# Optimization experiments

Measured on AMD Instinct MI355X. Metric: run time of the kernel, lower is better.

The kernel has to match this reference:

```python
import jax, jax.numpy as jnp
from jax import lax
import numpy as np

CH = 16      # channel_n
HID = 128    # update MLP width


def setup_inputs() -> dict:
    key = jax.random.key(0)
    ks = jax.random.split(key, 7)
    B, H, W = 4, 224, 224
    x = jax.random.uniform(ks[0], (B, CH, H, W), dtype=jnp.float32)
    # perception: Conv2d(16 -> 48, 3x3, pad 1, no bias), OIHW
    w_percep = jax.random.normal(ks[1], (CH * 3, CH, 3, 3), jnp.float32) * 0.05
    # update MLP: 1x1 convs == pointwise linears over channels
    w1 = jax.random.normal(ks[2], (HID, CH * 3), jnp.float32) * 0.05
    b1 = jax.random.normal(ks[3], (HID,), jnp.float32) * 0.01
    w2 = jax.random.normal(ks[4], (HID, HID), jnp.float32) * 0.05
    b2 = jax.random.normal(ks[5], (HID,), jnp.float32) * 0.01
    w3 = jax.random.normal(ks[6], (CH, HID), jnp.float32) * 0.05  # no bias
    return {"x": x, "w_percep": w_percep, "w1": w1, "b1": b1,
            "w2": w2, "b2": b2, "w3": w3, "steps": 40}


def reference(x, w_percep, w1, b1, w2, b2, w3, steps):
    dn = ("NCHW", "OIHW", "NCHW")

    def step(x, _):
        # 3x3 perception conv, same padding  -> [B, 48, H, W]
        p = lax.conv_general_dilated(x, w_percep, (1, 1), "SAME",
                                     dimension_numbers=dn)
        # pointwise conv-MLP (1x1 convs as channel einsums)
        h = jax.nn.relu(jnp.einsum("bchw,oc->bohw", p, w1) + b1[None, :, None, None])
        h = jax.nn.relu(jnp.einsum("bchw,oc->bohw", h, w2) + b2[None, :, None, None])
        dx = jnp.einsum("bchw,oc->bohw", h, w3)
        # residual update + clamp to [0, 1] (eval mode: no fire mask)
        return jnp.clip(x + dx, 0.0, 1.0), None

    x, _ = lax.scan(step, x, None, length=steps)
    return x
```

## Files before the change

### kernel.cpp

```cpp
#include <hip/hip_runtime.h>


typedef __attribute__((ext_vector_type(8))) short short8;
typedef __attribute__((ext_vector_type(4))) float float4v;
typedef __attribute__((ext_vector_type(2))) float float2v;

#define MFMA16(a, b, c) __builtin_amdgcn_mfma_f32_16x16x32_bf16((a), (b), (c), 0, 0, 0)

__device__ __forceinline__ short f2bf(float f) {
  unsigned u = __builtin_bit_cast(unsigned, f);
  return (short)((u + 0x8000u) >> 16);
}

__device__ __forceinline__ unsigned pk2bf(float a, float b) {
#if __has_builtin(__builtin_amdgcn_cvt_pk_bf16_f32)
  typedef __attribute__((ext_vector_type(2))) __bf16 bf2;
  bf2 r = __builtin_amdgcn_cvt_pk_bf16_f32(a, b);
  return __builtin_bit_cast(unsigned, r);
#else
  unsigned ua = __builtin_bit_cast(unsigned, a), ub = __builtin_bit_cast(unsigned, b);
  return ((ua + 0x8000u) >> 16) | (((ub + 0x8000u) >> 16) << 16);
#endif
}

__device__ __forceinline__ void async16(const void* g, void* l) {
  __builtin_amdgcn_global_load_lds((const __attribute__((address_space(1))) void*)g,
                                   (__attribute__((address_space(3))) void*)l,
                                   16, 0, 0);
}

__device__ __forceinline__ void sync_lds() {
  asm volatile("s_waitcnt lgkmcnt(0)\n\ts_barrier" ::: "memory");
}

#define WS_WE    0
#define WS_W2    43008
#define WS_W3    77824
#define WS_B1    82944
#define WS_B2    83456
#define WS_X32A  83968
#define WS_X32B  12929024
#define WS_X16A  25774080
#define WS_X16B  32196608

__global__ void prep_x(const float* __restrict__ x, float* __restrict__ x32,
                       short* __restrict__ x16) {
  int i = blockIdx.x * 256 + threadIdx.x;
  int w = i % 224;
  int h = (i / 224) % 224;
  int c = (i / 50176) & 15;
  int bb = i / 802816;
  float v = x[i];
  int o = ((bb * 224 + h) * 224 + w) * 16 + c;
  x32[o] = v;
  x16[o] = f2bf(v);
}

__global__ void prep_w(const float* __restrict__ wp, const float* __restrict__ w1,
                       const float* __restrict__ b1, const float* __restrict__ w2,
                       const float* __restrict__ b2, const float* __restrict__ w3,
                       short* __restrict__ wE, short* __restrict__ w2t,
                       short* __restrict__ w3t, float* __restrict__ b1p,
                       float* __restrict__ b2p) {
  int i = blockIdx.x * 256 + threadIdx.x;
  if (i < 21504) {
    int o = i / 168, k = i % 168;
    float v = 0.f;
    if (k < 144) {
      int off = k >> 4, c = k & 15;
      for (int c3 = 0; c3 < 48; ++c3)
        v += w1[o * 48 + c3] * wp[c3 * 144 + c * 9 + off];
    }
    wE[i] = f2bf(v);
  } else if (i < 38912) {
    int j = i - 21504;
    int n = j / 136, kk = j % 136;
    float v = 0.f;
    if (kk < 128) { int ch = 16 * (kk & 7) + (kk >> 3); v = w2[n * 128 + ch]; }
    w2t[j] = f2bf(v);
  } else if (i < 41472) {
    int j = i - 38912;
    float v = 0.f;
    if (j < 2176) {
      int n = j / 136, kk = j % 136;
      if (kk < 128) { int ch = 16 * (kk & 7) + (kk >> 3); v = w3[n * 128 + ch]; }
    }
    w3t[j] = f2bf(v);
  } else if (i < 41600) {
    int p = i - 41472;
    b1p[p] = b1[16 * (p & 7) + (p >> 3)];
  } else {
    int p = i - 41600;
    b2p[p] = b2[16 * (p & 7) + (p >> 3)];
  }
}

template <bool LAST>
__global__ __launch_bounds__(512, 4) void ca_step(
    const short* __restrict__ wEg, const short* __restrict__ w2g,
    const short* __restrict__ w3g, const float* __restrict__ b1p,
    const float* __restrict__ b2p, const float* __restrict__ xs32,
    const short* __restrict__ xs16, float* __restrict__ xd32,
    short* __restrict__ xd16, float* __restrict__ dout) {
  __shared__ short sXH[4 * 3616];
  __shared__ short sBUF[2 * 2 * 2176];
  __shared__ short sH2[2 * 2 * 2176];

  const int tid = threadIdx.x;
  const int lane = tid & 63;
  const int wv = tid >> 6;
  const int c16 = lane & 15;
  const int q = lane >> 4;
  const int q8 = q * 8;
  const int qh = q >> 1;
  const int c0 = (q & 1) * 8;

  const int blk = blockIdx.x;
  const int b = blk / 112;
  const int h0 = (blk % 112) * 2;

  const short8 z8 = {0, 0, 0, 0, 0, 0, 0, 0};
  for (int t = wv; t < 28; t += 8) {
    int hr = t / 7, ck = t % 7;
    int hh = h0 - 1 + hr;
    char* l = (char*)sXH + hr * 7232 + 32 + ck * 1024;
    if (hh >= 0 && hh < 224) {
      const char* g = (const char*)xs16 + ((size_t)(b * 224 + hh) * 224) * 32 + ck * 1024;
      async16(g + lane * 16, l);
    } else {
      *(short8*)(l + lane * 16) = z8;
    }
  }
  if (tid < 16) {
    int hr = tid >> 2, wch = tid & 3;
    int colb = (wch < 2) ? 0 : 225;
    *(short8*)((char*)sXH + hr * 7232 + colb * 32 + (wch & 1) * 16) = z8;
  }

  if (wv < 4) {
    const int wq = wv;
    short8 wf[5][2];
#pragma unroll
    for (int kc = 0; kc < 5; ++kc)
#pragma unroll
      for (int n = 0; n < 2; ++n)
        wf[kc][n] = *(const short8*)(wEg + ((2 * wq + n) * 16 + c16) * 168 + kc * 32 + q8);
    const float2v bH = *(const float2v*)(b1p + c16 * 8 + 2 * wq);

    __syncthreads();

    for (int j = 0; j < 16; ++j) {
      if (j < 14) {
        const int t0 = 2 * j, t1 = t0 + 1;
        const int hb0 = ((t0 / 14) * 226 + (t0 % 14) * 16) * 16;
        const int hb1 = ((t1 / 14) * 226 + (t1 % 14) * 16) * 16;
        float4v acc[2][2];
#pragma unroll
        for (int tt = 0; tt < 2; ++tt)
#pragma unroll
          for (int n = 0; n < 2; ++n) acc[tt][n] = (float4v){0.f, 0.f, 0.f, 0.f};
#pragma unroll
        for (int kc = 0; kc < 5; ++kc) {
          int off = kc * 2 + qh;
          if (off > 8) off = 8;
          int dy = (off * 11) >> 5;
          int dxx = off - dy * 3;
          const int ao = (dy * 226 + dxx + c16) * 16 + c0;
          short8 a0 = *(const short8*)(sXH + hb0 + ao);
          short8 a1 = *(const short8*)(sXH + hb1 + ao);
#pragma unroll
          for (int n = 0; n < 2; ++n) {
            acc[0][n] = MFMA16(a0, wf[kc][n], acc[0][n]);
            acc[1][n] = MFMA16(a1, wf[kc][n], acc[1][n]);
          }
        }
#pragma unroll
        for (int tt = 0; tt < 2; ++tt) {
          short* dst = sBUF + ((j & 1) * 2 + tt) * 2176;
#pragma unroll
          for (int r = 0; r < 4; ++r) {
            unsigned d = pk2bf(fmaxf(acc[tt][0][r] + bH[0], 0.f),
                               fmaxf(acc[tt][1][r] + bH[1], 0.f));
            *(unsigned*)(dst + (q * 4 + r) * 136 + c16 * 8 + 2 * wq) = d;
          }
        }
      }
      sync_lds();
    }
  } else {
    const int g = wv - 4;
    short8 w2f[4][2];
    short8 w3f[4];
#pragma unroll
    for (int kc = 0; kc < 4; ++kc)
#pragma unroll
      for (int n = 0; n < 2; ++n)
        w2f[kc][n] = *(const short8*)(w2g + ((2 * g + n) * 16 + c16) * 136 + kc * 32 + q8);
#pragma unroll
    for (int kc = 0; kc < 4; ++kc)
      w3f[kc] = *(const short8*)(w3g + c16 * 136 + kc * 32 + q8);
    const float2v bG = *(const float2v*)(b2p + c16 * 8 + 2 * g);

    __syncthreads();

    for (int j = 0; j < 16; ++j) {
      float xres[4];
      int cb3 = 0, hglob3 = 0;
      if (g < 2 && j >= 2) {
        const int t3 = 2 * (j - 2) + g;
        cb3 = (t3 % 14) * 16; hglob3 = h0 + t3 / 14;
#pragma unroll
        for (int r = 0; r < 4; ++r) {
          size_t pix = (size_t)(b * 224 + hglob3) * 224 + cb3 + q * 4 + r;
          xres[r] = xs32[pix * 16 + c16];
        }
      }
      if (j >= 1 && j <= 14) {
        const short* srcA = sBUF + (((j - 1) & 1) * 2 + 0) * 2176;
        const short* srcB = sBUF + (((j - 1) & 1) * 2 + 1) * 2176;
        float4v acc2[2][2];
#pragma unroll
        for (int tt = 0; tt < 2; ++tt)
#pragma unroll
          for (int n = 0; n < 2; ++n) acc2[tt][n] = (float4v){0.f, 0.f, 0.f, 0.f};
#pragma unroll
        for (int kc = 0; kc < 4; ++kc) {
          short8 aA = *(const short8*)(srcA + c16 * 136 + kc * 32 + q8);
          short8 aB = *(const short8*)(srcB + c16 * 136 + kc * 32 + q8);
#pragma unroll
          for (int n = 0; n < 2; ++n) {
            acc2[0][n] = MFMA16(aA, w2f[kc][n], acc2[0][n]);
            acc2[1][n] = MFMA16(aB, w2f[kc][n], acc2[1][n]);
          }
        }
#pragma unroll
        for (int tt = 0; tt < 2; ++tt) {
          short* dsth2 = sH2 + ((j & 1) * 2 + tt) * 2176;
#pragma unroll
          for (int r = 0; r < 4; ++r) {
            unsigned d = pk2bf(fmaxf(acc2[tt][0][r] + bG[0], 0.f),
                               fmaxf(acc2[tt][1][r] + bG[1], 0.f));
            *(unsigned*)(dsth2 + (q * 4 + r) * 136 + c16 * 8 + 2 * g) = d;
          }
        }
      }
      if (g < 2 && j >= 2) {
        const short* srch2 = sH2 + (((j - 1) & 1) * 2 + g) * 2176;
        float4v acc3 = (float4v){0.f, 0.f, 0.f, 0.f};
#pragma unroll
        for (int kc = 0; kc < 4; ++kc) {
          short8 a = *(const short8*)(srch2 + c16 * 136 + kc * 32 + q8);
          acc3 = MFMA16(a, w3f[kc], acc3);
        }
#pragma unroll
        for (int r = 0; r < 4; ++r) {
          int col = cb3 + q * 4 + r;
          size_t pix = (size_t)(b * 224 + hglob3) * 224 + col;
          float v = xres[r] + acc3[r];
          v = fminf(fmaxf(v, 0.f), 1.f);
          if (LAST) {
            dout[((size_t)(b * 16 + c16) * 224 + hglob3) * 224 + col] = v;
          } else {
            xd32[pix * 16 + c16] = v;
            xd16[pix * 16 + c16] = f2bf(v);
          }
        }
      }
      sync_lds();
    }
  }
}

extern "C" void kernel_launch(void* const* d_in, const int* in_sizes, int n_in,
                              void* d_out, int out_size, void* d_ws, size_t ws_size,
                              hipStream_t stream) {
  const float* x  = (const float*)d_in[0];
  const float* wp = (const float*)d_in[1];
  const float* w1 = (const float*)d_in[2];
  const float* b1 = (const float*)d_in[3];
  const float* w2 = (const float*)d_in[4];
  const float* b2 = (const float*)d_in[5];
  const float* w3 = (const float*)d_in[6];

  char* ws = (char*)d_ws;
  short* wEg = (short*)(ws + WS_WE);
  short* w2g = (short*)(ws + WS_W2);
  short* w3g = (short*)(ws + WS_W3);
  float* b1p = (float*)(ws + WS_B1);
  float* b2p = (float*)(ws + WS_B2);
  float* X32[2] = {(float*)(ws + WS_X32A), (float*)(ws + WS_X32B)};
  short* X16[2] = {(short*)(ws + WS_X16A), (short*)(ws + WS_X16B)};

  prep_x<<<12544, 256, 0, stream>>>(x, X32[0], X16[0]);
  prep_w<<<163, 256, 0, stream>>>(wp, w1, b1, w2, b2, w3, wEg, w2g, w3g, b1p, b2p);

  for (int s = 0; s < 39; ++s) {
    int sb = s & 1;
    ca_step<false><<<448, 512, 0, stream>>>(wEg, w2g, w3g, b1p, b2p,
                                            X32[sb], X16[sb],
                                            X32[1 - sb], X16[1 - sb], nullptr);
  }
  ca_step<true><<<448, 512, 0, stream>>>(wEg, w2g, w3g, b1p, b2p,
                                         X32[1], X16[1],
                                         X32[0], X16[0], (float*)d_out);
}
```

Measured before the change: 1.007 ms.

## Pipeline one 16-pixel tile per stage instead of two, halving LDS buffers

Each producer and consumer stage now handles a single 16-pixel tile per iteration, running 30 pipeline iterations instead of 16, and the layer-1 and layer-2 staging buffers shrink by half. The final w3 layer rotates among all four consumer warps (one per iteration) instead of being done by two warps on paired tiles. This cuts LDS use and register pressure and balances layer-3 work, which may allow higher occupancy. The cost is roughly twice as many block-wide LDS barriers and less MFMA work per barrier to hide latency.

```diff
diff --git a/kernel.cpp b/kernel.cpp
--- a/kernel.cpp
+++ b/kernel.cpp
@@ -103,8 +103,8 @@
     const short* __restrict__ xs16, float* __restrict__ xd32,
     short* __restrict__ xd16, float* __restrict__ dout) {
   __shared__ short sXH[4 * 3616];
-  __shared__ short sBUF[2 * 2 * 2176];
-  __shared__ short sH2[2 * 2 * 2176];
+  __shared__ short sBUF[2 * 2176];
+  __shared__ short sH2[2 * 2176];
 
   const int tid = threadIdx.x;
   const int lane = tid & 63;
@@ -149,40 +149,28 @@
 
     __syncthreads();
 
-    for (int j = 0; j < 16; ++j) {
-      if (j < 14) {
-        const int t0 = 2 * j, t1 = t0 + 1;
-        const int hb0 = ((t0 / 14) * 226 + (t0 % 14) * 16) * 16;
-        const int hb1 = ((t1 / 14) * 226 + (t1 % 14) * 16) * 16;
-        float4v acc[2][2];
-#pragma unroll
-        for (int tt = 0; tt < 2; ++tt)
-#pragma unroll
-          for (int n = 0; n < 2; ++n) acc[tt][n] = (float4v){0.f, 0.f, 0.f, 0.f};
+    for (int j = 0; j < 30; ++j) {
+      if (j < 28) {
+        const int hb = ((j / 14) * 226 + (j % 14) * 16) * 16;
+        float4v acc[2];
+        acc[0] = (float4v){0.f, 0.f, 0.f, 0.f};
+        acc[1] = (float4v){0.f, 0.f, 0.f, 0.f};
 #pragma unroll
         for (int kc = 0; kc < 5; ++kc) {
           int off = kc * 2 + qh;
           if (off > 8) off = 8;
           int dy = (off * 11) >> 5;
           int dxx = off - dy * 3;
-          const int ao = (dy * 226 + dxx + c16) * 16 + c0;
-          short8 a0 = *(const short8*)(sXH + hb0 + ao);
-          short8 a1 = *(const short8*)(sXH + hb1 + ao);
-#pragma unroll
-          for (int n = 0; n < 2; ++n) {
-            acc[0][n] = MFMA16(a0, wf[kc][n], acc[0][n]);
-            acc[1][n] = MFMA16(a1, wf[kc][n], acc[1][n]);
-          }
-        }
-#pragma unroll
-        for (int tt = 0; tt < 2; ++tt) {
-          short* dst = sBUF + ((j & 1) * 2 + tt) * 2176;
-#pragma unroll
-          for (int r = 0; r < 4; ++r) {
-            unsigned d = pk2bf(fmaxf(acc[tt][0][r] + bH[0], 0.f),
-                               fmaxf(acc[tt][1][r] + bH[1], 0.f));
-            *(unsigned*)(dst + (q * 4 + r) * 136 + c16 * 8 + 2 * wq) = d;
-          }
+          short8 a = *(const short8*)(sXH + hb + (dy * 226 + dxx + c16) * 16 + c0);
+          acc[0] = MFMA16(a, wf[kc][0], acc[0]);
+          acc[1] = MFMA16(a, wf[kc][1], acc[1]);
+        }
+        short* dst = sBUF + (j & 1) * 2176;
+#pragma unroll
+        for (int r = 0; r < 4; ++r) {
+          unsigned d = pk2bf(fmaxf(acc[0][r] + bH[0], 0.f),
+                             fmaxf(acc[1][r] + bH[1], 0.f));
+          *(unsigned*)(dst + (q * 4 + r) * 136 + c16 * 8 + 2 * wq) = d;
         }
       }
       sync_lds();
@@ -203,11 +191,12 @@
 
     __syncthreads();
 
-    for (int j = 0; j < 16; ++j) {
+    for (int j = 0; j < 30; ++j) {
+      const bool own3 = (j >= 2) && (((j - 2) & 3) == g);
       float xres[4];
       int cb3 = 0, hglob3 = 0;
-      if (g < 2 && j >= 2) {
-        const int t3 = 2 * (j - 2) + g;
+      if (own3) {
+        const int t3 = j - 2;
         cb3 = (t3 % 14) * 16; hglob3 = h0 + t3 / 14;
 #pragma unroll
         for (int r = 0; r < 4; ++r) {
@@ -215,37 +204,27 @@
           xres[r] = xs32[pix * 16 + c16];
         }
       }
-      if (j >= 1 && j <= 14) {
-        const short* srcA = sBUF + (((j - 1) & 1) * 2 + 0) * 2176;
-        const short* srcB = sBUF + (((j - 1) & 1) * 2 + 1) * 2176;
-        float4v acc2[2][2];
-#pragma unroll
-        for (int tt = 0; tt < 2; ++tt)
-#pragma unroll
-          for (int n = 0; n < 2; ++n) acc2[tt][n] = (float4v){0.f, 0.f, 0.f, 0.f};
+      if (j >= 1 && j <= 28) {
+        const short* src = sBUF + ((j - 1) & 1) * 2176;
+        float4v acc2[2];
+        acc2[0] = (float4v){0.f, 0.f, 0.f, 0.f};
+        acc2[1] = (float4v){0.f, 0.f, 0.f, 0.f};
 #pragma unroll
         for (int kc = 0; kc < 4; ++kc) {
-          short8 aA = *(const short8*)(srcA + c16 * 136 + kc * 32 + q8);
-          short8 aB = *(const short8*)(srcB + c16 * 136 + kc * 32 + q8);
-#pragma unroll
-          for (int n = 0; n < 2; ++n) {
-            acc2[0][n] = MFMA16(aA, w2f[kc][n], acc2[0][n]);
-            acc2[1][n] = MFMA16(aB, w2f[kc][n], acc2[1][n]);
-          }
-        }
-#pragma unroll
-        for (int tt = 0; tt < 2; ++tt) {
-          short* dsth2 = sH2 + ((j & 1) * 2 + tt) * 2176;
-#pragma unroll
-          for (int r = 0; r < 4; ++r) {
-            unsigned d = pk2bf(fmaxf(acc2[tt][0][r] + bG[0], 0.f),
-                               fmaxf(acc2[tt][1][r] + bG[1], 0.f));
-            *(unsigned*)(dsth2 + (q * 4 + r) * 136 + c16 * 8 + 2 * g) = d;
-          }
-        }
-      }
-      if (g < 2 && j >= 2) {
-        const short* srch2 = sH2 + (((j - 1) & 1) * 2 + g) * 2176;
+          short8 a = *(const short8*)(src + c16 * 136 + kc * 32 + q8);
+          acc2[0] = MFMA16(a, w2f[kc][0], acc2[0]);
+          acc2[1] = MFMA16(a, w2f[kc][1], acc2[1]);
+        }
+        short* dsth2 = sH2 + (j & 1) * 2176;
+#pragma unroll
+        for (int r = 0; r < 4; ++r) {
+          unsigned d = pk2bf(fmaxf(acc2[0][r] + bG[0], 0.f),
+                             fmaxf(acc2[1][r] + bG[1], 0.f));
+          *(unsigned*)(dsth2 + (q * 4 + r) * 136 + c16 * 8 + 2 * g) = d;
+        }
+      }
+      if (own3) {
+        const short* srch2 = sH2 + ((j - 1) & 1) * 2176;
         float4v acc3 = (float4v){0.f, 0.f, 0.f, 0.f};
 #pragma unroll
         for (int kc = 0; kc < 4; ++kc) {
```

Result: slower. 1.185 ms (+17.7%).
